# Kernel tuning notes

Measured on AMD Instinct MI355X. Metric: run time of the kernel, lower is better.

## Reference

```python
import jax, jax.numpy as jnp
import numpy as np

B, L = 4096, 2048
TAU = 0.85        # DivLoss tau (augmented=True)
MARGIN = 0.0005   # RerankLoss margin
RW = 0.5          # rerank_weight
CW = 0.5          # classi_weight


def setup_inputs() -> dict:
    key = jax.random.key(0)
    k1, k2, k3, k4 = jax.random.split(key, 4)
    # cut_y: per-row probability distribution over L cut positions (softmax output)
    cut_y = jax.nn.softmax(jax.random.normal(k1, (B, L)), axis=1)[..., None]
    # pred_y: sigmoid-like probabilities in (0,1) for BCE
    pred_y = jax.random.uniform(k2, (B, L, 1)) * 0.98 + 0.01
    rerank_y = jax.random.normal(k3, (B, L, 1))
    labels = jax.random.randint(k4, (B, L), 0, 2).astype(jnp.float32)
    return {"pred_y": pred_y, "rerank_y": rerank_y, "cut_y": cut_y, "labels": labels}


def _kl_batchmean(target, log_input):
    # torch.nn.KLDivLoss(reduction='batchmean'): sum(target*(log target - log_input)) / B
    term = jnp.where(target > 0, target * (jnp.log(jnp.where(target > 0, target, 1.0)) - log_input), 0.0)
    return jnp.sum(term) / target.shape[0]


def reference(pred_y, rerank_y, cut_y, labels):
    Bn, Ln = labels.shape
    # ---- DivLoss (metric='f1', div_type='js', augmented=True) ----
    # Vectorized replacement of the per-element double loop:
    # f1 at cut k: p = c/k, r = c/T -> 2*c/(k+T) where c = #relevant in top-k
    c = jnp.cumsum(labels, axis=1)                     # [B,L] prefix relevant counts
    T = c[:, -1:]                                      # [B,1] total relevant per row
    k = jnp.arange(1, Ln + 1, dtype=labels.dtype)      # cut positions 1..L
    r = 2.0 * c / (k[None, :] + T)                     # f1 reward per cut position
    q = jax.nn.softmax(r / TAU, axis=1)                # q = exp(r/tau)/sum
    p = cut_y[..., 0]                                  # output.squeeze()
    log_mean = jnp.log((p + q) * 0.5)
    cutloss = 0.5 * (_kl_batchmean(q, log_mean) + _kl_batchmean(p, log_mean))
    # ---- RerankLoss (hinge on mean pos vs mean neg scores) ----
    s = rerank_y[..., 0]
    pos = (labels == 1.0)
    neg = (labels == 0.0)
    pos_mean = jnp.sum(jnp.where(pos, s, 0.0)) / jnp.sum(pos)
    neg_mean = jnp.sum(jnp.where(neg, s, 0.0)) / jnp.sum(neg)
    rerankloss = jnp.maximum(0.0, neg_mean - pos_mean + MARGIN) * RW
    # ---- BCELoss ----
    pp = pred_y[..., 0]
    bce = -jnp.mean(labels * jnp.log(pp) + (1.0 - labels) * jnp.log(1.0 - pp)) * CW
    return cutloss + rerankloss + bce
```

## Files before the change

kernel.cpp:

```cpp
#include <hip/hip_runtime.h>

namespace {
constexpr int Bn = 4096;
constexpr int Ln = 2048;
constexpr float TAU = 0.85f;
constexpr float MARGIN = 0.0005f;
constexpr float RW = 0.5f;
constexpr float CW = 0.5f;

constexpr int RPB = 4;
constexpr int EPL = Ln / 64;
static_assert(EPL == 32, "layout assumption");

typedef float f32x4 __attribute__((ext_vector_type(4)));

__global__ __launch_bounds__(256) void mt_row_kernel(
    const float* __restrict__ pred,
    const float* __restrict__ rerank,
    const float* __restrict__ cut,
    const float* __restrict__ labels,
    float* __restrict__ part)
{
  const int tid  = threadIdx.x;
  const int lane = tid & 63;
  const int wid  = tid >> 6;
  const int row  = blockIdx.x * RPB + wid;
  const size_t base = (size_t)row * Ln + (size_t)lane * EPL;
  const float* __restrict__ lrow = labels + base;
  const float* __restrict__ yrow = pred   + base;
  const float* __restrict__ srow = rerank + base;
  const float* __restrict__ prow = cut    + base;

  unsigned mask = 0u;
  float bce = 0.f, s_all = 0.f, s_pos = 0.f;
  #pragma unroll
  for (int c = 0; c < 8; ++c) {
    const f32x4 lv = *(const f32x4*)(lrow + 4 * c);
    const f32x4 yv = *(const f32x4*)(yrow + 4 * c);
    const f32x4 sv = *(const f32x4*)(srow + 4 * c);
    #pragma unroll
    for (int u = 0; u < 4; ++u) {
      const int j = 4 * c + u;
      const bool pos = (lv[u] == 1.f);
      mask  |= (pos ? 1u : 0u) << j;
      bce   += __logf(pos ? yv[u] : 1.f - yv[u]);
      s_all += sv[u];
      s_pos += pos ? sv[u] : 0.f;
    }
  }

  const float own = (float)__builtin_popcount(mask);
  float sc = own;
  #pragma unroll
  for (int off = 1; off < 64; off <<= 1) {
    const float n = __shfl_up(sc, off, 64);
    if (lane >= off) sc += n;
  }
  const float T    = __shfl(sc, 63, 64);
  const float excl = sc - own;

  float esum0 = 0.f, esum1 = 0.f, t1a = 0.f, t1b = 0.f;
  int ci = 0;
  const float kbase = (float)(lane * EPL);
  #pragma unroll
  for (int j = 0; j < EPL; ++j) {
    ci += (int)((mask >> j) & 1u);
    const float cf = excl + (float)ci;
    const float k  = kbase + (float)(j + 1);
    const float z  = __fdividef(2.f * cf, (k + T) * TAU);
    const float ev = __expf(z);
    if (j & 1) { esum1 += ev; t1b += ev * z; }
    else       { esum0 += ev; t1a += ev * z; }
  }
  float esum = esum0 + esum1;
  float t1   = t1a + t1b;

  #pragma unroll
  for (int off = 32; off > 0; off >>= 1) {
    esum += __shfl_xor(esum, off, 64);
    t1   += __shfl_xor(t1,   off, 64);
  }
  const float inv = 1.f / esum;

  float kl = 0.f;
  ci = 0;
  #pragma unroll
  for (int c = 0; c < 8; ++c) {
    const f32x4 pv = *(const f32x4*)(prow + 4 * c);
    #pragma unroll
    for (int u = 0; u < 4; ++u) {
      const int j = 4 * c + u;
      ci += (int)((mask >> j) & 1u);
      const float cf = excl + (float)ci;
      const float k  = kbase + (float)(j + 1);
      const float z  = __fdividef(2.f * cf, (k + T) * TAU);
      const float q  = __expf(z) * inv;
      const float p  = pv[u];
      const float pq = p + q;
      kl += p * __logf(p) - pq * __logf(pq * 0.5f);
    }
  }

  #pragma unroll
  for (int off = 32; off > 0; off >>= 1) {
    kl    += __shfl_xor(kl,    off, 64);
    s_all += __shfl_xor(s_all, off, 64);
    s_pos += __shfl_xor(s_pos, off, 64);
    bce   += __shfl_xor(bce,   off, 64);
  }
  if (lane == 0) {
    part[0 * Bn + row] = kl + t1 * inv - __logf(esum);
    part[1 * Bn + row] = s_all;
    part[2 * Bn + row] = s_pos;
    part[3 * Bn + row] = bce;
    part[4 * Bn + row] = T;
  }
}

__global__ __launch_bounds__(256) void mt_final_kernel(
    const float* __restrict__ part, float* __restrict__ out)
{
  const int tid  = threadIdx.x;
  const int lane = tid & 63;
  const int wid  = tid >> 6;
  double kl = 0, sv = 0, sp = 0, bc = 0, tt = 0;
  for (int r = tid; r < Bn; r += 256) {
    kl += (double)part[0 * Bn + r];
    sv += (double)part[1 * Bn + r];
    sp += (double)part[2 * Bn + r];
    bc += (double)part[3 * Bn + r];
    tt += (double)part[4 * Bn + r];
  }
  #pragma unroll
  for (int off = 32; off > 0; off >>= 1) {
    kl += __shfl_xor(kl, off, 64);
    sv += __shfl_xor(sv, off, 64);
    sp += __shfl_xor(sp, off, 64);
    bc += __shfl_xor(bc, off, 64);
    tt += __shfl_xor(tt, off, 64);
  }
  __shared__ double sh[4][5];
  if (lane == 0) { sh[wid][0] = kl; sh[wid][1] = sv; sh[wid][2] = sp; sh[wid][3] = bc; sh[wid][4] = tt; }
  __syncthreads();
  if (tid == 0) {
    kl = sh[0][0] + sh[1][0] + sh[2][0] + sh[3][0];
    sv = sh[0][1] + sh[1][1] + sh[2][1] + sh[3][1];
    sp = sh[0][2] + sh[1][2] + sh[2][2] + sh[3][2];
    bc = sh[0][3] + sh[1][3] + sh[2][3] + sh[3][3];
    tt = sh[0][4] + sh[1][4] + sh[2][4] + sh[3][4];
    const double total = (double)Bn * (double)Ln;
    const double posc = tt, negc = total - tt;
    double rer = (sv - sp) / negc - sp / posc + (double)MARGIN;
    if (rer < 0.0) rer = 0.0;
    rer *= (double)RW;
    const double cutl = 0.5 * kl / (double)Bn;
    const double bcel = -(bc / total) * (double)CW;
    out[0] = (float)(cutl + rer + bcel);
  }
}
}

extern "C" void kernel_launch(void* const* d_in, const int* in_sizes, int n_in,
                              void* d_out, int out_size, void* d_ws, size_t ws_size,
                              hipStream_t stream) {
  const float* pred   = (const float*)d_in[0];
  const float* rerank = (const float*)d_in[1];
  const float* cut    = (const float*)d_in[2];
  const float* labels = (const float*)d_in[3];
  float* part = (float*)d_ws;
  mt_row_kernel<<<Bn / RPB, 256, 0, stream>>>(pred, rerank, cut, labels, part);
  mt_final_kernel<<<1, 256, 0, stream>>>(part, (float*)d_out);
}
```

Before: 182.3 us.

## Interleave row elements across lanes for coalesced loads, use ballot-based prefix counts

Each lane now reads a strided float4 chunk (256 floats per wave step) rather than a contiguous 32-element block, so a wave's global loads are fully coalesced. The per-lane prefix sum over contiguous chunks is replaced by ballot/mbcnt counts for each of the 4 sub-positions in every 256-element segment, plus a running segment base. The total relevant count now comes from an xor-reduction. This adds many ballot and mbcnt instructions in both passes in exchange for better memory access patterns.

```diff
diff --git a/kernel.cpp b/kernel.cpp
--- a/kernel.cpp
+++ b/kernel.cpp
@@ -9,10 +9,15 @@
 constexpr float CW = 0.5f;
 
 constexpr int RPB = 4;
-constexpr int EPL = Ln / 64;
-static_assert(EPL == 32, "layout assumption");
+constexpr int NSC = Ln / 256;
+static_assert(NSC == 8, "layout assumption");
 
 typedef float f32x4 __attribute__((ext_vector_type(4)));
+
+__device__ __forceinline__ int mbcnt64(unsigned long long m) {
+  return (int)__builtin_amdgcn_mbcnt_hi((unsigned)(m >> 32),
+              __builtin_amdgcn_mbcnt_lo((unsigned)m, 0u));
+}
 
 __global__ __launch_bounds__(256) void mt_row_kernel(
     const float* __restrict__ pred,
@@ -25,56 +30,57 @@
   const int lane = tid & 63;
   const int wid  = tid >> 6;
   const int row  = blockIdx.x * RPB + wid;
-  const size_t base = (size_t)row * Ln + (size_t)lane * EPL;
-  const float* __restrict__ lrow = labels + base;
-  const float* __restrict__ yrow = pred   + base;
-  const float* __restrict__ srow = rerank + base;
-  const float* __restrict__ prow = cut    + base;
+  const size_t rbase = (size_t)row * Ln;
+  const int l4 = lane * 4;
 
   unsigned mask = 0u;
   float bce = 0.f, s_all = 0.f, s_pos = 0.f;
   #pragma unroll
-  for (int c = 0; c < 8; ++c) {
-    const f32x4 lv = *(const f32x4*)(lrow + 4 * c);
-    const f32x4 yv = *(const f32x4*)(yrow + 4 * c);
-    const f32x4 sv = *(const f32x4*)(srow + 4 * c);
+  for (int J = 0; J < NSC; ++J) {
+    const size_t off = rbase + (size_t)(J * 256 + l4);
+    const f32x4 lv = *(const f32x4*)(labels + off);
+    const f32x4 yv = *(const f32x4*)(pred   + off);
+    const f32x4 sv = *(const f32x4*)(rerank + off);
     #pragma unroll
     for (int u = 0; u < 4; ++u) {
-      const int j = 4 * c + u;
       const bool pos = (lv[u] == 1.f);
-      mask  |= (pos ? 1u : 0u) << j;
+      mask  |= (pos ? 1u : 0u) << (4 * J + u);
       bce   += __logf(pos ? yv[u] : 1.f - yv[u]);
       s_all += sv[u];
       s_pos += pos ? sv[u] : 0.f;
     }
   }
 
-  const float own = (float)__builtin_popcount(mask);
-  float sc = own;
+  int tot = __builtin_popcount(mask);
   #pragma unroll
-  for (int off = 1; off < 64; off <<= 1) {
-    const float n = __shfl_up(sc, off, 64);
-    if (lane >= off) sc += n;
+  for (int off = 32; off > 0; off >>= 1) tot += __shfl_xor(tot, off, 64);
+  const float T = (float)tot;
+
+  float esum = 0.f, t1 = 0.f;
+  int base = 0;
+  #pragma unroll
+  for (int J = 0; J < NSC; ++J) {
+    int cnt_lt = 0, totJ = 0;
+    #pragma unroll
+    for (int u = 0; u < 4; ++u) {
+      const unsigned long long b = __ballot((mask >> (4 * J + u)) & 1u);
+      cnt_lt += mbcnt64(b);
+      totJ   += (int)__builtin_popcountll(b);
+    }
+    int p = 0;
+    const float kb = (float)(J * 256 + l4);
+    #pragma unroll
+    for (int u = 0; u < 4; ++u) {
+      p += (int)((mask >> (4 * J + u)) & 1u);
+      const float cf = (float)(base + cnt_lt + p);
+      const float k  = kb + (float)(u + 1);
+      const float z  = __fdividef(2.f * cf, (k + T) * TAU);
+      const float ev = __expf(z);
+      esum += ev;
+      t1   += ev * z;
+    }
+    base += totJ;
   }
-  const float T    = __shfl(sc, 63, 64);
-  const float excl = sc - own;
-
-  float esum0 = 0.f, esum1 = 0.f, t1a = 0.f, t1b = 0.f;
-  int ci = 0;
-  const float kbase = (float)(lane * EPL);
-  #pragma unroll
-  for (int j = 0; j < EPL; ++j) {
-    ci += (int)((mask >> j) & 1u);
-    const float cf = excl + (float)ci;
-    const float k  = kbase + (float)(j + 1);
-    const float z  = __fdividef(2.f * cf, (k + T) * TAU);
-    const float ev = __expf(z);
-    if (j & 1) { esum1 += ev; t1b += ev * z; }
-    else       { esum0 += ev; t1a += ev * z; }
-  }
-  float esum = esum0 + esum1;
-  float t1   = t1a + t1b;
-
   #pragma unroll
   for (int off = 32; off > 0; off >>= 1) {
     esum += __shfl_xor(esum, off, 64);
@@ -83,22 +89,32 @@
   const float inv = 1.f / esum;
 
   float kl = 0.f;
-  ci = 0;
+  base = 0;
   #pragma unroll
-  for (int c = 0; c < 8; ++c) {
-    const f32x4 pv = *(const f32x4*)(prow + 4 * c);
+  for (int J = 0; J < NSC; ++J) {
+    const size_t off = rbase + (size_t)(J * 256 + l4);
+    const f32x4 pv = *(const f32x4*)(cut + off);
+    int cnt_lt = 0, totJ = 0;
     #pragma unroll
     for (int u = 0; u < 4; ++u) {
-      const int j = 4 * c + u;
-      ci += (int)((mask >> j) & 1u);
-      const float cf = excl + (float)ci;
-      const float k  = kbase + (float)(j + 1);
+      const unsigned long long b = __ballot((mask >> (4 * J + u)) & 1u);
+      cnt_lt += mbcnt64(b);
+      totJ   += (int)__builtin_popcountll(b);
+    }
+    int p = 0;
+    const float kb = (float)(J * 256 + l4);
+    #pragma unroll
+    for (int u = 0; u < 4; ++u) {
+      p += (int)((mask >> (4 * J + u)) & 1u);
+      const float cf = (float)(base + cnt_lt + p);
+      const float k  = kb + (float)(u + 1);
       const float z  = __fdividef(2.f * cf, (k + T) * TAU);
       const float q  = __expf(z) * inv;
-      const float p  = pv[u];
-      const float pq = p + q;
-      kl += p * __logf(p) - pq * __logf(pq * 0.5f);
+      const float pp = pv[u];
+      const float pq = pp + q;
+      kl += pp * __logf(pp) - pq * __logf(pq * 0.5f);
     }
+    base += totJ;
   }
 
   #pragma unroll
```

Result: faster. 159.2 us (-12.7%).
